# Optimization experiments

Hardware: AMD Instinct MI355X
Metric: run time of the kernel (lower is better)

Reference implementation:

```python
import jax, jax.numpy as jnp
import numpy as np

N, H, D, HDIM, HID = 768, 4, 3, 64, 64


def setup_inputs() -> dict:
    key = jax.random.key(0)
    ks = jax.random.split(key, 12)

    def w(k, shape, scale=None):
        s = (1.0 / np.sqrt(shape[0])) if scale is None else scale
        return (jax.random.normal(k, shape, jnp.float32) * s).astype(jnp.float32)

    d_in_e = H + 2 * (HDIM + H * H)  # 4 + 2*(64+16) = 164
    return {
        "x": jax.random.normal(ks[0], (N, H, D), jnp.float32),
        "h": jax.random.normal(ks[1], (N, HDIM), jnp.float32),
        "phi_e_w0": w(ks[2], (d_in_e, HID)), "phi_e_b0": jnp.zeros((HID,), jnp.float32),
        "phi_e_w1": w(ks[3], (HID, HID)), "phi_e_b1": jnp.zeros((HID,), jnp.float32),
        "phi_inf_w": w(ks[4], (HID, 1)), "phi_inf_b": jnp.zeros((1,), jnp.float32),
        "phi_x_w0": w(ks[5], (HID, HID)), "phi_x_b0": jnp.zeros((HID,), jnp.float32),
        "phi_x_w1": w(ks[6], (HID, HID)), "phi_x_b1": jnp.zeros((HID,), jnp.float32),
        "phi_x_w2": w(ks[7], (HID, H), scale=0.001), "phi_x_b2": jnp.zeros((H,), jnp.float32),
        "phi_h_w0": w(ks[8], (HID + HDIM, HID)), "phi_h_b0": jnp.zeros((HID,), jnp.float32),
        "phi_h_w1": w(ks[9], (HID, HID)), "phi_h_b1": jnp.zeros((HID,), jnp.float32),
        "phi_h_w2": w(ks[10], (HID, HDIM)), "phi_h_b2": jnp.zeros((HDIM,), jnp.float32),
    }


def _mlp2(z, w0, b0, w1, b1):
    # hk.nets.MLP([HID, HID], activation=silu, activate_final=True)
    return jax.nn.silu(jax.nn.silu(z @ w0 + b0) @ w1 + b1)


def reference(x, h,
              phi_e_w0, phi_e_b0, phi_e_w1, phi_e_b1,
              phi_inf_w, phi_inf_b,
              phi_x_w0, phi_x_b0, phi_x_w1, phi_x_b1, phi_x_w2, phi_x_b2,
              phi_h_w0, phi_h_b0, phi_h_w1, phi_h_b1, phi_h_w2, phi_h_b2):
    n, n_heads = x.shape[0], x.shape[1]
    avg_num_neighbours = n - 1
    off_n = 1.0 - jnp.eye(n, dtype=x.dtype)          # zero node-diagonal mask

    # per-node head-pair differences: [n, H, H, 3], entry [m,i,j] = x[m,j]-x[m,i]
    diff_heads = x[:, None, :, :] - x[:, :, None, :]
    sq_norms_heads = jnp.sum(diff_heads ** 2, axis=-1)            # [n, H, H]
    h_concat = jnp.concatenate([h, sq_norms_heads.reshape(n, n_heads * n_heads)], axis=-1)

    # all-pairs node features: [n, n, 2*(HDIM+H^2)], entry [i,j] = [h_concat[j], h_concat[i]]
    hc_dim = h_concat.shape[-1]
    h_combos = jnp.concatenate([
        jnp.broadcast_to(h_concat[None, :, :], (n, n, hc_dim)),
        jnp.broadcast_to(h_concat[:, None, :], (n, n, hc_dim)),
    ], axis=-1)

    # all-pairs node differences per head: [n, n, H, 3], entry [i,j] = x[j]-x[i]
    diff_nodes = x[None, :, :, :] - x[:, None, :, :]
    sq_norms_nodes = jnp.sum(diff_nodes ** 2, axis=-1)            # [n, n, H]

    e_in = jnp.concatenate([sq_norms_nodes, h_combos], axis=-1)   # [n, n, 164]
    m_ij = _mlp2(e_in, phi_e_w0, phi_e_b0, phi_e_w1, phi_e_b1)    # [n, n, HID]
    m_ij = m_ij * off_n[:, :, None]

    e = jax.nn.sigmoid(m_ij @ phi_inf_w + phi_inf_b)[..., 0] * off_n  # [n, n]
    m_i = jnp.einsum('ijd,ij->id', m_ij, e) / jnp.sqrt(jnp.asarray(avg_num_neighbours, x.dtype))

    # phi_x: MLP(silu, activate_final) -> Linear(H) (tanh=False)
    phi_x_out = (_mlp2(m_ij, phi_x_w0, phi_x_b0, phi_x_w1, phi_x_b1) @ phi_x_w2 + phi_x_b2)
    phi_x_out = phi_x_out * off_n[:, :, None]                     # [n, n, H]

    # normalize_by_x_norm=True, normalization_constant=1.0
    norm = jnp.sqrt(jnp.where(sq_norms_nodes == 0.0, 1.0, sq_norms_nodes)) + 1.0
    norm_diff = (diff_nodes / norm[..., None]) * off_n[:, :, None, None]
    equivariant_shift = jnp.einsum('ijhd,ijh->ihd', norm_diff, phi_x_out)
    equivariant_shift = equivariant_shift / avg_num_neighbours    # agg='mean'

    x_new = x + equivariant_shift

    phi_h_in = jnp.concatenate([m_i, h], axis=-1)
    h_new = _mlp2(phi_h_in, phi_h_w0, phi_h_b0, phi_h_w1, phi_h_b1) @ phi_h_w2 + phi_h_b2
    h_new = h + h_new                                             # residual_h=True
    return (x_new, h_new)
```

## Files before the change

### kernel.cpp

```cpp
#include <hip/hip_runtime.h>
#include <hip/hip_bf16.h>
#include <math.h>

#define WS_BJ    0
#define WS_BI    49152
#define WS_W0AT  98304
#define WS_BIAS  98560
#define WS_INFW  98784
#define WS_WG    98848

typedef unsigned short ushort_t;
typedef __attribute__((ext_vector_type(8))) __bf16 bf16x8;
typedef __attribute__((ext_vector_type(4))) float f32x4;

__device__ __forceinline__ float silu_f(float v) {
    return v * __builtin_amdgcn_rcpf(1.0f + __expf(-v));
}
__device__ __forceinline__ float sigm_f(float v) {
    return __builtin_amdgcn_rcpf(1.0f + __expf(-v));
}

__device__ __forceinline__ ushort_t bf16r(float f) {
    unsigned u = __float_as_uint(f);
    u += 0x7FFFu + ((u >> 16) & 1u);
    return (ushort_t)(u >> 16);
}
__device__ __forceinline__ float bf2f(ushort_t s) { return __uint_as_float(((unsigned)s) << 16); }

__device__ __forceinline__ unsigned pk2(float a, float b) {
    __hip_bfloat162 t = __float22bfloat162_rn(make_float2(a, b));
    return *reinterpret_cast<unsigned*>(&t);
}

__global__ __launch_bounds__(64) void prep_kernel(
    const float* __restrict__ x, const float* __restrict__ h,
    const float* __restrict__ ew0, const float* __restrict__ eb0,
    const float* __restrict__ ew1, const float* __restrict__ eb1,
    const float* __restrict__ infw, const float* __restrict__ infb,
    const float* __restrict__ xw0, const float* __restrict__ xb0,
    const float* __restrict__ xw1, const float* __restrict__ xb1,
    const float* __restrict__ xw2, const float* __restrict__ xb2,
    float* __restrict__ ws)
{
    const int blk = blockIdx.x, t = threadIdx.x;
    if (blk < 768) {
        __shared__ float hcs[80];
        const int m = blk;
        hcs[t] = h[m * 64 + t];
        if (t < 16) {
            int i2 = t >> 2, j2 = t & 3;
            float d0 = x[m*12 + j2*3 + 0] - x[m*12 + i2*3 + 0];
            float d1 = x[m*12 + j2*3 + 1] - x[m*12 + i2*3 + 1];
            float d2 = x[m*12 + j2*3 + 2] - x[m*12 + i2*3 + 2];
            hcs[64 + t] = d0*d0 + d1*d1 + d2*d2;
        }
        __syncthreads();
        float bj = 0.0f, bi = eb0[t];
        #pragma unroll 4
        for (int k = 0; k < 80; ++k) {
            float hv = hcs[k];
            bj += hv * ew0[(4 + k) * 64 + t];
            bi += hv * ew0[(84 + k) * 64 + t];
        }
        ws[WS_BJ + m * 64 + t] = bj;
        ws[WS_BI + m * 64 + t] = bi;
    } else if (blk == 768) {
        #pragma unroll
        for (int hh = 0; hh < 4; ++hh) ws[WS_W0AT + t * 4 + hh] = ew0[hh * 64 + t];
        ws[WS_INFW + t] = infw[t];
        #pragma unroll
        for (int u = 0; u < 4; ++u) {
            int idx = u * 64 + t;
            if (idx < 224) {
                float v;
                if (idx < 64)        v = eb1[idx];
                else if (idx < 128)  v = xb0[idx - 64];
                else if (idx == 128) v = infb[0];
                else if (idx < 144)  v = 0.0f;
                else if (idx < 208)  v = xb1[idx - 144];
                else if (idx < 212)  v = xb2[idx - 208];
                else                 v = 0.0f;
                ws[WS_BIAS + idx] = v;
            }
        }
    } else {
        ushort_t* wg = (ushort_t*)(ws + WS_WG);
        #pragma unroll 1
        for (int u = 0; u < 8; ++u) {
            int e = (blk - 769) * 512 + u * 64 + t;
            int r = e >> 6, k = e & 63;
            float v;
            if (r < 64)        v = ew1[k * 64 + r];
            else if (r < 128)  v = xw0[k * 64 + (r - 64)];
            else if (r == 128) v = infw[k];
            else if (r < 144)  v = 0.0f;
            else if (r < 208)  v = xw1[k * 64 + (r - 144)];
            else if (r < 212)  v = xw2[k * 4 + (r - 208)];
            else               v = 0.0f;
            wg[e] = bf16r(v);
        }
    }
}

__device__ __forceinline__ void load_bfrags(const ushort_t* yb, int ml, int q, bf16x8 B[4][2]) {
    #pragma unroll
    for (int pt = 0; pt < 4; ++pt)
        #pragma unroll
        for (int kt = 0; kt < 2; ++kt)
            B[pt][kt] = *(const bf16x8*)(yb + (pt*16 + ml) * 72 + kt*32 + q*8);
}

template<int NMT>
__device__ __forceinline__ void gemmG(const ushort_t* __restrict__ wg, int ml, int q,
                                      const bf16x8 B[4][2], f32x4* acc) {
    #pragma unroll
    for (int mt = 0; mt < NMT; ++mt) {
        #pragma unroll
        for (int kt = 0; kt < 2; ++kt) {
            bf16x8 af = *(const bf16x8*)(wg + (mt*16 + ml) * 64 + kt*32 + q*8);
            #pragma unroll
            for (int pt = 0; pt < 4; ++pt)
                acc[mt*4 + pt] = __builtin_amdgcn_mfma_f32_16x16x32_bf16(af, B[pt][kt], acc[mt*4 + pt], 0, 0, 0);
        }
    }
}

__device__ __forceinline__ void ep_silu2(ushort_t* yb, int ml, int q,
                                         const f32x4* acc, const float* __restrict__ bias,
                                         int coff) {
    #pragma unroll
    for (int mt = 0; mt < 2; ++mt) {
        float4 bv = *(const float4*)(bias + coff + mt*16 + q*4);
        #pragma unroll
        for (int pt = 0; pt < 4; ++pt) {
            f32x4 a = acc[mt*4 + pt];
            uint2 w = make_uint2(pk2(silu_f(a[0] + bv.x), silu_f(a[1] + bv.y)),
                                 pk2(silu_f(a[2] + bv.z), silu_f(a[3] + bv.w)));
            *(uint2*)(yb + (pt*16 + ml) * 72 + coff + mt*16 + q*4) = w;
        }
    }
}

__device__ __forceinline__ void layer64(ushort_t* yb, const ushort_t* __restrict__ wg,
                                        const float* __restrict__ bias, int ml, int q) {
    bf16x8 B[4][2];
    load_bfrags(yb, ml, q, B);
    f32x4 acc[8];
    #pragma unroll
    for (int t = 0; t < 8; ++t) acc[t] = f32x4{0.f, 0.f, 0.f, 0.f};
    gemmG<2>(wg, ml, q, B, acc);
    ep_silu2(yb, ml, q, acc, bias, 0);
    #pragma unroll
    for (int t = 0; t < 8; ++t) acc[t] = f32x4{0.f, 0.f, 0.f, 0.f};
    gemmG<2>(wg + 32*64, ml, q, B, acc);
    ep_silu2(yb, ml, q, acc, bias, 32);
}

__global__ __launch_bounds__(256, 2) void egcl_kernel(
    const float* __restrict__ x, const float* __restrict__ h,
    const float* __restrict__ hw0, const float* __restrict__ hb0,
    const float* __restrict__ hw1, const float* __restrict__ hb1,
    const float* __restrict__ hw2, const float* __restrict__ hb2,
    const float* __restrict__ ws, float* __restrict__ out)
{
    __shared__ ushort_t ybuf[4][4608];
    __shared__ float sbuf[4][64];
    __shared__ float pbuf[4][256];
    __shared__ float redm[4][64];
    __shared__ float reds[4][12];
    __shared__ float inbuf[128];
    __shared__ float zbuf[64];

    const int i = blockIdx.x, tid = threadIdx.x;
    const int wv = tid >> 6, lane = tid & 63;
    const int ml = lane & 15, q = lane >> 4;

    const ushort_t* wg = (const ushort_t*)(ws + WS_WG);
    const float* bias  = ws + WS_BIAS;
    const float* infwf = ws + WS_INFW;

    if (wv == 1) inbuf[64 + lane] = h[i * 64 + lane];
    if (lane < 12) reds[wv][lane] = 0.0f;

    float xi[12];
    #pragma unroll
    for (int t = 0; t < 12; ++t) xi[t] = x[i * 12 + t];

    const float* Bi   = ws + WS_BI + i * 64;
    const float* w0at = ws + WS_W0AT;
    ushort_t* yb = ybuf[wv];

    float macc = 0.0f;

    #pragma unroll 1
    for (int it = 0; it < 3; ++it) {
        const int jg = it * 256 + wv * 64 + lane;

        float sqn[4];
        {
            const float4* xp = (const float4*)(x + jg * 12);
            float4 a = xp[0], b = xp[1], c = xp[2];
            float d0, d1, d2;
            d0=a.x-xi[0]; d1=a.y-xi[1]; d2=a.z-xi[2];   sqn[0]=d0*d0+d1*d1+d2*d2;
            d0=a.w-xi[3]; d1=b.x-xi[4]; d2=b.y-xi[5];   sqn[1]=d0*d0+d1*d1+d2*d2;
            d0=b.z-xi[6]; d1=b.w-xi[7]; d2=c.x-xi[8];   sqn[2]=d0*d0+d1*d1+d2*d2;
            d0=c.y-xi[9]; d1=c.z-xi[10];d2=c.w-xi[11];  sqn[3]=d0*d0+d1*d1+d2*d2;
        }

        {
            const float* Bj = ws + WS_BJ + jg * 64;
            #pragma unroll
            for (int b = 0; b < 8; ++b) {
                float4 A = *(const float4*)(Bj + b*8);
                float4 Bv = *(const float4*)(Bj + b*8 + 4);
                float z[8] = {A.x, A.y, A.z, A.w, Bv.x, Bv.y, Bv.z, Bv.w};
                #pragma unroll
                for (int u = 0; u < 8; ++u) {
                    int l = b*8 + u;
                    float v = Bi[l] + z[u]
                            + sqn[0]*w0at[l*4+0] + sqn[1]*w0at[l*4+1]
                            + sqn[2]*w0at[l*4+2] + sqn[3]*w0at[l*4+3];
                    z[u] = silu_f(v);
                }
                uint4 pkv = make_uint4(pk2(z[0],z[1]), pk2(z[2],z[3]),
                                       pk2(z[4],z[5]), pk2(z[6],z[7]));
                *(uint4*)(yb + lane * 72 + b*8) = pkv;
            }
        }

        layer64(yb, wg + 0, bias + 0, ml, q);

        {
            float sv = bias[128];
            #pragma unroll
            for (int c = 0; c < 8; ++c) {
                uint2 w0 = *(const uint2*)(yb + lane * 72 + c*8);
                uint2 w1 = *(const uint2*)(yb + lane * 72 + c*8 + 4);
                sv += __uint_as_float(w0.x << 16)          * infwf[c*8 + 0];
                sv += __uint_as_float(w0.x & 0xFFFF0000u)  * infwf[c*8 + 1];
                sv += __uint_as_float(w0.y << 16)          * infwf[c*8 + 2];
                sv += __uint_as_float(w0.y & 0xFFFF0000u)  * infwf[c*8 + 3];
                sv += __uint_as_float(w1.x << 16)          * infwf[c*8 + 4];
                sv += __uint_as_float(w1.x & 0xFFFF0000u)  * infwf[c*8 + 5];
                sv += __uint_as_float(w1.y << 16)          * infwf[c*8 + 6];
                sv += __uint_as_float(w1.y & 0xFFFF0000u)  * infwf[c*8 + 7];
            }
            sbuf[wv][lane] = (jg == i) ? 0.0f : sigm_f(sv);
        }

        #pragma unroll 8
        for (int j2 = 0; j2 < 64; ++j2) {
            float ev = sbuf[wv][j2];
            macc += ev * bf2f(yb[j2 * 72 + lane]);
        }

        layer64(yb, wg + 64*64, bias + 64, ml, q);
        layer64(yb, wg + 144*64, bias + 144, ml, q);

        {
            bf16x8 B[4][2];
            load_bfrags(yb, ml, q, B);
            f32x4 acc2[4];
            #pragma unroll
            for (int t = 0; t < 4; ++t) acc2[t] = f32x4{0.f, 0.f, 0.f, 0.f};
            gemmG<1>(wg + 208*64, ml, q, B, acc2);
            if (q == 0) {
                float4 bx2 = *(const float4*)(bias + 208);
                #pragma unroll
                for (int pt = 0; pt < 4; ++pt) {
                    float4 pv = make_float4(acc2[pt][0] + bx2.x, acc2[pt][1] + bx2.y,
                                            acc2[pt][2] + bx2.z, acc2[pt][3] + bx2.w);
                    *(float4*)(pbuf[wv] + (pt*16 + ml) * 4) = pv;
                }
            }
        }

        {
            float4 pv = *(const float4*)(pbuf[wv] + lane * 4);
            float pvh[4] = {pv.x, pv.y, pv.z, pv.w};
            float mask = (jg == i) ? 0.0f : 1.0f;
            const float4* xp = (const float4*)(x + jg * 12);
            float4 a = xp[0], b = xp[1], c = xp[2];
            float dxs[12];
            dxs[0]=a.x-xi[0]; dxs[1]=a.y-xi[1]; dxs[2]=a.z-xi[2];  dxs[3]=a.w-xi[3];
            dxs[4]=b.x-xi[4]; dxs[5]=b.y-xi[5]; dxs[6]=b.z-xi[6];  dxs[7]=b.w-xi[7];
            dxs[8]=c.x-xi[8]; dxs[9]=c.y-xi[9]; dxs[10]=c.z-xi[10];dxs[11]=c.w-xi[11];
            float s12[12];
            #pragma unroll
            for (int hh = 0; hh < 4; ++hh) {
                float nsq = (sqn[hh] == 0.0f) ? 1.0f : sqn[hh];
                float inv = mask * pvh[hh] * __builtin_amdgcn_rcpf(sqrtf(nsq) + 1.0f);
                #pragma unroll
                for (int d = 0; d < 3; ++d)
                    s12[hh*3 + d] = dxs[hh*3 + d] * inv;
            }
            #pragma unroll
            for (int t = 0; t < 12; ++t) {
                float v = s12[t];
                v += __shfl_xor(v, 1, 64);
                v += __shfl_xor(v, 2, 64);
                v += __shfl_xor(v, 4, 64);
                v += __shfl_xor(v, 8, 64);
                v += __shfl_xor(v, 16, 64);
                v += __shfl_xor(v, 32, 64);
                if (lane == 0) reds[wv][t] += v;
            }
        }
    }

    redm[wv][lane] = macc;
    __syncthreads();

    if (wv == 0) {
        float mi = (redm[0][lane] + redm[1][lane] + redm[2][lane] + redm[3][lane])
                   * (1.0f / sqrtf(767.0f));
        inbuf[lane] = mi;

        if (lane < 12) {
            float sh = reds[0][lane] + reds[1][lane] + reds[2][lane] + reds[3][lane];
            out[i*12 + lane] = x[i*12 + lane] + sh * (1.0f / 767.0f);
        }

        float a = hb0[lane];
        #pragma unroll 8
        for (int k = 0; k < 128; ++k) a += inbuf[k] * hw0[k*64 + lane];
        zbuf[lane] = silu_f(a);

        a = hb1[lane];
        #pragma unroll 8
        for (int k = 0; k < 64; ++k) a += zbuf[k] * hw1[k*64 + lane];
        zbuf[lane] = silu_f(a);

        a = hb2[lane];
        #pragma unroll 8
        for (int k = 0; k < 64; ++k) a += zbuf[k] * hw2[k*64 + lane];
        out[9216 + i*64 + lane] = h[i*64 + lane] + a;
    }
}

extern "C" void kernel_launch(void* const* d_in, const int* in_sizes, int n_in,
                              void* d_out, int out_size, void* d_ws, size_t ws_size,
                              hipStream_t stream) {
    const float* x    = (const float*)d_in[0];
    const float* h    = (const float*)d_in[1];
    const float* ew0  = (const float*)d_in[2];
    const float* eb0  = (const float*)d_in[3];
    const float* ew1  = (const float*)d_in[4];
    const float* eb1  = (const float*)d_in[5];
    const float* infw = (const float*)d_in[6];
    const float* infb = (const float*)d_in[7];
    const float* xw0  = (const float*)d_in[8];
    const float* xb0  = (const float*)d_in[9];
    const float* xw1  = (const float*)d_in[10];
    const float* xb1  = (const float*)d_in[11];
    const float* xw2  = (const float*)d_in[12];
    const float* xb2  = (const float*)d_in[13];
    const float* hw0  = (const float*)d_in[14];
    const float* hb0  = (const float*)d_in[15];
    const float* hw1  = (const float*)d_in[16];
    const float* hb1  = (const float*)d_in[17];
    const float* hw2  = (const float*)d_in[18];
    const float* hb2  = (const float*)d_in[19];

    float* ws  = (float*)d_ws;
    float* out = (float*)d_out;

    prep_kernel<<<797, 64, 0, stream>>>(x, h, ew0, eb0, ew1, eb1, infw, infb,
                                        xw0, xb0, xw1, xb1, xw2, xb2, ws);
    egcl_kernel<<<768, 256, 0, stream>>>(x, h, hw0, hb0, hw1, hb1, hw2, hb2, ws, out);
}
```

Before: 203.8 us.

## Split per-node j-loop across blocks and move phi_h MLP to a finish kernel

The main kernel no longer loops three times over 256-neighbour chunks within one block. It launches a 3x768 grid where each block handles one chunk and writes partial m_i and shift sums to workspace. A separate finish kernel reduces the partials and runs the phi_h MLP. The prep kernel is repacked into 256-thread blocks with four nodes each, and the weight-packing store pattern changes. This triples the block count for better CU occupancy and load balance, and takes the serial single-wave tail out of the heavy kernel, at the cost of an extra launch and a workspace round-trip.

```diff
diff --git a/kernel.cpp b/kernel.cpp
--- a/kernel.cpp
+++ b/kernel.cpp
@@ -8,6 +8,8 @@
 #define WS_BIAS  98560
 #define WS_INFW  98784
 #define WS_WG    98848
+#define WS_PM    106016
+#define WS_PS    253472
 
 typedef unsigned short ushort_t;
 typedef __attribute__((ext_vector_type(8))) __bf16 bf16x8;
@@ -32,7 +34,7 @@
     return *reinterpret_cast<unsigned*>(&t);
 }
 
-__global__ __launch_bounds__(64) void prep_kernel(
+__global__ __launch_bounds__(256) void prep_kernel(
     const float* __restrict__ x, const float* __restrict__ h,
     const float* __restrict__ ew0, const float* __restrict__ eb0,
     const float* __restrict__ ew1, const float* __restrict__ eb1,
@@ -42,52 +44,54 @@
     const float* __restrict__ xw2, const float* __restrict__ xb2,
     float* __restrict__ ws)
 {
-    const int blk = blockIdx.x, t = threadIdx.x;
-    if (blk < 768) {
-        __shared__ float hcs[80];
-        const int m = blk;
-        hcs[t] = h[m * 64 + t];
+    const int blk = blockIdx.x, tid = threadIdx.x;
+    const int wv = tid >> 6, t = tid & 63;
+    if (blk < 192) {
+        __shared__ float hcs[4][80];
+        const int m = blk * 4 + wv;
+        hcs[wv][t] = h[m * 64 + t];
         if (t < 16) {
             int i2 = t >> 2, j2 = t & 3;
             float d0 = x[m*12 + j2*3 + 0] - x[m*12 + i2*3 + 0];
             float d1 = x[m*12 + j2*3 + 1] - x[m*12 + i2*3 + 1];
             float d2 = x[m*12 + j2*3 + 2] - x[m*12 + i2*3 + 2];
-            hcs[64 + t] = d0*d0 + d1*d1 + d2*d2;
-        }
-        __syncthreads();
+            hcs[wv][64 + t] = d0*d0 + d1*d1 + d2*d2;
+        }
         float bj = 0.0f, bi = eb0[t];
         #pragma unroll 4
         for (int k = 0; k < 80; ++k) {
-            float hv = hcs[k];
+            float hv = hcs[wv][k];
             bj += hv * ew0[(4 + k) * 64 + t];
             bi += hv * ew0[(84 + k) * 64 + t];
         }
         ws[WS_BJ + m * 64 + t] = bj;
         ws[WS_BI + m * 64 + t] = bi;
-    } else if (blk == 768) {
-        #pragma unroll
-        for (int hh = 0; hh < 4; ++hh) ws[WS_W0AT + t * 4 + hh] = ew0[hh * 64 + t];
-        ws[WS_INFW + t] = infw[t];
-        #pragma unroll
-        for (int u = 0; u < 4; ++u) {
-            int idx = u * 64 + t;
-            if (idx < 224) {
-                float v;
-                if (idx < 64)        v = eb1[idx];
-                else if (idx < 128)  v = xb0[idx - 64];
-                else if (idx == 128) v = infb[0];
-                else if (idx < 144)  v = 0.0f;
-                else if (idx < 208)  v = xb1[idx - 144];
-                else if (idx < 212)  v = xb2[idx - 208];
-                else                 v = 0.0f;
-                ws[WS_BIAS + idx] = v;
+    } else if (blk == 192) {
+        if (wv == 0) {
+            #pragma unroll
+            for (int hh = 0; hh < 4; ++hh) ws[WS_W0AT + t * 4 + hh] = ew0[hh * 64 + t];
+            ws[WS_INFW + t] = infw[t];
+            #pragma unroll
+            for (int u = 0; u < 4; ++u) {
+                int idx = u * 64 + t;
+                if (idx < 224) {
+                    float v;
+                    if (idx < 64)        v = eb1[idx];
+                    else if (idx < 128)  v = xb0[idx - 64];
+                    else if (idx == 128) v = infb[0];
+                    else if (idx < 144)  v = 0.0f;
+                    else if (idx < 208)  v = xb1[idx - 144];
+                    else if (idx < 212)  v = xb2[idx - 208];
+                    else                 v = 0.0f;
+                    ws[WS_BIAS + idx] = v;
+                }
             }
         }
     } else {
         ushort_t* wg = (ushort_t*)(ws + WS_WG);
         #pragma unroll 1
         for (int u = 0; u < 8; ++u) {
-            int e = (blk - 769) * 512 + u * 64 + t;
+            int e = (blk - 193) * 2048 + tid * 8 + u;
             int r = e >> 6, k = e & 63;
             float v;
             if (r < 64)        v = ew1[k * 64 + r];
@@ -156,186 +160,191 @@
     ep_silu2(yb, ml, q, acc, bias, 32);
 }
 
-__global__ __launch_bounds__(256, 2) void egcl_kernel(
+__global__ __launch_bounds__(256, 2) void egcl_chunk(
+    const float* __restrict__ x, float* __restrict__ ws)
+{
+    __shared__ ushort_t ybuf[4][4608];
+    __shared__ float sbuf[4][64];
+    __shared__ float redm[4][64];
+    __shared__ float reds[4][12];
+
+    const int it = blockIdx.x, i = blockIdx.y, tid = threadIdx.x;
+    const int wv = tid >> 6, lane = tid & 63;
+    const int ml = lane & 15, q = lane >> 4;
+    const int jg = it * 256 + wv * 64 + lane;
+
+    const ushort_t* wg = (const ushort_t*)(ws + WS_WG);
+    const float* bias  = ws + WS_BIAS;
+    const float* infwf = ws + WS_INFW;
+    const float* Bi    = ws + WS_BI + i * 64;
+    const float* w0at  = ws + WS_W0AT;
+    ushort_t* yb = ybuf[wv];
+
+    float xi[12];
+    #pragma unroll
+    for (int t = 0; t < 12; ++t) xi[t] = x[i * 12 + t];
+
+    float sqn[4];
+    {
+        const float4* xp = (const float4*)(x + jg * 12);
+        float4 a = xp[0], b = xp[1], c = xp[2];
+        float d0, d1, d2;
+        d0=a.x-xi[0]; d1=a.y-xi[1]; d2=a.z-xi[2];   sqn[0]=d0*d0+d1*d1+d2*d2;
+        d0=a.w-xi[3]; d1=b.x-xi[4]; d2=b.y-xi[5];   sqn[1]=d0*d0+d1*d1+d2*d2;
+        d0=b.z-xi[6]; d1=b.w-xi[7]; d2=c.x-xi[8];   sqn[2]=d0*d0+d1*d1+d2*d2;
+        d0=c.y-xi[9]; d1=c.z-xi[10];d2=c.w-xi[11];  sqn[3]=d0*d0+d1*d1+d2*d2;
+    }
+
+    {
+        const float* Bj = ws + WS_BJ + jg * 64;
+        #pragma unroll
+        for (int b = 0; b < 8; ++b) {
+            float4 A = *(const float4*)(Bj + b*8);
+            float4 Bv = *(const float4*)(Bj + b*8 + 4);
+            float z[8] = {A.x, A.y, A.z, A.w, Bv.x, Bv.y, Bv.z, Bv.w};
+            #pragma unroll
+            for (int u = 0; u < 8; ++u) {
+                int l = b*8 + u;
+                float v = Bi[l] + z[u]
+                        + sqn[0]*w0at[l*4+0] + sqn[1]*w0at[l*4+1]
+                        + sqn[2]*w0at[l*4+2] + sqn[3]*w0at[l*4+3];
+                z[u] = silu_f(v);
+            }
+            uint4 pkv = make_uint4(pk2(z[0],z[1]), pk2(z[2],z[3]),
+                                   pk2(z[4],z[5]), pk2(z[6],z[7]));
+            *(uint4*)(yb + lane * 72 + b*8) = pkv;
+        }
+    }
+
+    layer64(yb, wg + 0, bias + 0, ml, q);
+
+    {
+        float sv = bias[128];
+        #pragma unroll
+        for (int c = 0; c < 8; ++c) {
+            uint2 w0 = *(const uint2*)(yb + lane * 72 + c*8);
+            uint2 w1 = *(const uint2*)(yb + lane * 72 + c*8 + 4);
+            sv += __uint_as_float(w0.x << 16)          * infwf[c*8 + 0];
+            sv += __uint_as_float(w0.x & 0xFFFF0000u)  * infwf[c*8 + 1];
+            sv += __uint_as_float(w0.y << 16)          * infwf[c*8 + 2];
+            sv += __uint_as_float(w0.y & 0xFFFF0000u)  * infwf[c*8 + 3];
+            sv += __uint_as_float(w1.x << 16)          * infwf[c*8 + 4];
+            sv += __uint_as_float(w1.x & 0xFFFF0000u)  * infwf[c*8 + 5];
+            sv += __uint_as_float(w1.y << 16)          * infwf[c*8 + 6];
+            sv += __uint_as_float(w1.y & 0xFFFF0000u)  * infwf[c*8 + 7];
+        }
+        sbuf[wv][lane] = (jg == i) ? 0.0f : sigm_f(sv);
+    }
+
+    float macc = 0.0f;
+    #pragma unroll 8
+    for (int j2 = 0; j2 < 64; ++j2) {
+        float ev = sbuf[wv][j2];
+        macc += ev * bf2f(yb[j2 * 72 + lane]);
+    }
+
+    layer64(yb, wg + 64*64, bias + 64, ml, q);
+    layer64(yb, wg + 144*64, bias + 144, ml, q);
+
+    float* yf = (float*)yb;
+    {
+        bf16x8 B[4][2];
+        load_bfrags(yb, ml, q, B);
+        f32x4 acc2[4];
+        #pragma unroll
+        for (int t = 0; t < 4; ++t) acc2[t] = f32x4{0.f, 0.f, 0.f, 0.f};
+        gemmG<1>(wg + 208*64, ml, q, B, acc2);
+        if (q == 0) {
+            float4 bx2 = *(const float4*)(bias + 208);
+            #pragma unroll
+            for (int pt = 0; pt < 4; ++pt) {
+                float4 pv = make_float4(acc2[pt][0] + bx2.x, acc2[pt][1] + bx2.y,
+                                        acc2[pt][2] + bx2.z, acc2[pt][3] + bx2.w);
+                *(float4*)(yf + (pt*16 + ml) * 4) = pv;
+            }
+        }
+    }
+
+    {
+        float4 pv = *(const float4*)(yf + lane * 4);
+        float pvh[4] = {pv.x, pv.y, pv.z, pv.w};
+        float mask = (jg == i) ? 0.0f : 1.0f;
+        const float4* xp = (const float4*)(x + jg * 12);
+        float4 a = xp[0], b = xp[1], c = xp[2];
+        float dxs[12];
+        dxs[0]=a.x-xi[0]; dxs[1]=a.y-xi[1]; dxs[2]=a.z-xi[2];  dxs[3]=a.w-xi[3];
+        dxs[4]=b.x-xi[4]; dxs[5]=b.y-xi[5]; dxs[6]=b.z-xi[6];  dxs[7]=b.w-xi[7];
+        dxs[8]=c.x-xi[8]; dxs[9]=c.y-xi[9]; dxs[10]=c.z-xi[10];dxs[11]=c.w-xi[11];
+        float s12[12];
+        #pragma unroll
+        for (int hh = 0; hh < 4; ++hh) {
+            float nsq = (sqn[hh] == 0.0f) ? 1.0f : sqn[hh];
+            float inv = mask * pvh[hh] * __builtin_amdgcn_rcpf(sqrtf(nsq) + 1.0f);
+            #pragma unroll
+            for (int d = 0; d < 3; ++d)
+                s12[hh*3 + d] = dxs[hh*3 + d] * inv;
+        }
+        #pragma unroll
+        for (int t = 0; t < 12; ++t) {
+            float v = s12[t];
+            v += __shfl_xor(v, 1, 64);
+            v += __shfl_xor(v, 2, 64);
+            v += __shfl_xor(v, 4, 64);
+            v += __shfl_xor(v, 8, 64);
+            v += __shfl_xor(v, 16, 64);
+            v += __shfl_xor(v, 32, 64);
+            if (lane == 0) reds[wv][t] = v;
+        }
+    }
+
+    redm[wv][lane] = macc;
+    __syncthreads();
+
+    if (wv == 0) {
+        ws[WS_PM + (i*3 + it)*64 + lane] =
+            redm[0][lane] + redm[1][lane] + redm[2][lane] + redm[3][lane];
+        if (lane < 12)
+            ws[WS_PS + (i*3 + it)*12 + lane] =
+                reds[0][lane] + reds[1][lane] + reds[2][lane] + reds[3][lane];
+    }
+}
+
+__global__ __launch_bounds__(64) void finish_kernel(
     const float* __restrict__ x, const float* __restrict__ h,
     const float* __restrict__ hw0, const float* __restrict__ hb0,
     const float* __restrict__ hw1, const float* __restrict__ hb1,
     const float* __restrict__ hw2, const float* __restrict__ hb2,
     const float* __restrict__ ws, float* __restrict__ out)
 {
-    __shared__ ushort_t ybuf[4][4608];
-    __shared__ float sbuf[4][64];
-    __shared__ float pbuf[4][256];
-    __shared__ float redm[4][64];
-    __shared__ float reds[4][12];
     __shared__ float inbuf[128];
     __shared__ float zbuf[64];
-
-    const int i = blockIdx.x, tid = threadIdx.x;
-    const int wv = tid >> 6, lane = tid & 63;
-    const int ml = lane & 15, q = lane >> 4;
-
-    const ushort_t* wg = (const ushort_t*)(ws + WS_WG);
-    const float* bias  = ws + WS_BIAS;
-    const float* infwf = ws + WS_INFW;
-
-    if (wv == 1) inbuf[64 + lane] = h[i * 64 + lane];
-    if (lane < 12) reds[wv][lane] = 0.0f;
-
-    float xi[12];
-    #pragma unroll
-    for (int t = 0; t < 12; ++t) xi[t] = x[i * 12 + t];
-
-    const float* Bi   = ws + WS_BI + i * 64;
-    const float* w0at = ws + WS_W0AT;
-    ushort_t* yb = ybuf[wv];
-
-    float macc = 0.0f;
-
-    #pragma unroll 1
-    for (int it = 0; it < 3; ++it) {
-        const int jg = it * 256 + wv * 64 + lane;
-
-        float sqn[4];
-        {
-            const float4* xp = (const float4*)(x + jg * 12);
-            float4 a = xp[0], b = xp[1], c = xp[2];
-            float d0, d1, d2;
-            d0=a.x-xi[0]; d1=a.y-xi[1]; d2=a.z-xi[2];   sqn[0]=d0*d0+d1*d1+d2*d2;
-            d0=a.w-xi[3]; d1=b.x-xi[4]; d2=b.y-xi[5];   sqn[1]=d0*d0+d1*d1+d2*d2;
-            d0=b.z-xi[6]; d1=b.w-xi[7]; d2=c.x-xi[8];   sqn[2]=d0*d0+d1*d1+d2*d2;
-            d0=c.y-xi[9]; d1=c.z-xi[10];d2=c.w-xi[11];  sqn[3]=d0*d0+d1*d1+d2*d2;
-        }
-
-        {
-            const float* Bj = ws + WS_BJ + jg * 64;
-            #pragma unroll
-            for (int b = 0; b < 8; ++b) {
-                float4 A = *(const float4*)(Bj + b*8);
-                float4 Bv = *(const float4*)(Bj + b*8 + 4);
-                float z[8] = {A.x, A.y, A.z, A.w, Bv.x, Bv.y, Bv.z, Bv.w};
-                #pragma unroll
-                for (int u = 0; u < 8; ++u) {
-                    int l = b*8 + u;
-                    float v = Bi[l] + z[u]
-                            + sqn[0]*w0at[l*4+0] + sqn[1]*w0at[l*4+1]
-                            + sqn[2]*w0at[l*4+2] + sqn[3]*w0at[l*4+3];
-                    z[u] = silu_f(v);
-                }
-                uint4 pkv = make_uint4(pk2(z[0],z[1]), pk2(z[2],z[3]),
-                                       pk2(z[4],z[5]), pk2(z[6],z[7]));
-                *(uint4*)(yb + lane * 72 + b*8) = pkv;
-            }
-        }
-
-        layer64(yb, wg + 0, bias + 0, ml, q);
-
-        {
-            float sv = bias[128];
-            #pragma unroll
-            for (int c = 0; c < 8; ++c) {
-                uint2 w0 = *(const uint2*)(yb + lane * 72 + c*8);
-                uint2 w1 = *(const uint2*)(yb + lane * 72 + c*8 + 4);
-                sv += __uint_as_float(w0.x << 16)          * infwf[c*8 + 0];
-                sv += __uint_as_float(w0.x & 0xFFFF0000u)  * infwf[c*8 + 1];
-                sv += __uint_as_float(w0.y << 16)          * infwf[c*8 + 2];
-                sv += __uint_as_float(w0.y & 0xFFFF0000u)  * infwf[c*8 + 3];
-                sv += __uint_as_float(w1.x << 16)          * infwf[c*8 + 4];
-                sv += __uint_as_float(w1.x & 0xFFFF0000u)  * infwf[c*8 + 5];
-                sv += __uint_as_float(w1.y << 16)          * infwf[c*8 + 6];
-                sv += __uint_as_float(w1.y & 0xFFFF0000u)  * infwf[c*8 + 7];
-            }
-            sbuf[wv][lane] = (jg == i) ? 0.0f : sigm_f(sv);
-        }
-
-        #pragma unroll 8
-        for (int j2 = 0; j2 < 64; ++j2) {
-            float ev = sbuf[wv][j2];
-            macc += ev * bf2f(yb[j2 * 72 + lane]);
-        }
-
-        layer64(yb, wg + 64*64, bias + 64, ml, q);
-        layer64(yb, wg + 144*64, bias + 144, ml, q);
-
-        {
-            bf16x8 B[4][2];
-            load_bfrags(yb, ml, q, B);
-            f32x4 acc2[4];
-            #pragma unroll
-            for (int t = 0; t < 4; ++t) acc2[t] = f32x4{0.f, 0.f, 0.f, 0.f};
-            gemmG<1>(wg + 208*64, ml, q, B, acc2);
-            if (q == 0) {
-                float4 bx2 = *(const float4*)(bias + 208);
-                #pragma unroll
-                for (int pt = 0; pt < 4; ++pt) {
-                    float4 pv = make_float4(acc2[pt][0] + bx2.x, acc2[pt][1] + bx2.y,
-                                            acc2[pt][2] + bx2.z, acc2[pt][3] + bx2.w);
-                    *(float4*)(pbuf[wv] + (pt*16 + ml) * 4) = pv;
-                }
-            }
-        }
-
-        {
-            float4 pv = *(const float4*)(pbuf[wv] + lane * 4);
-            float pvh[4] = {pv.x, pv.y, pv.z, pv.w};
-            float mask = (jg == i) ? 0.0f : 1.0f;
-            const float4* xp = (const float4*)(x + jg * 12);
-            float4 a = xp[0], b = xp[1], c = xp[2];
-            float dxs[12];
-            dxs[0]=a.x-xi[0]; dxs[1]=a.y-xi[1]; dxs[2]=a.z-xi[2];  dxs[3]=a.w-xi[3];
-            dxs[4]=b.x-xi[4]; dxs[5]=b.y-xi[5]; dxs[6]=b.z-xi[6];  dxs[7]=b.w-xi[7];
-            dxs[8]=c.x-xi[8]; dxs[9]=c.y-xi[9]; dxs[10]=c.z-xi[10];dxs[11]=c.w-xi[11];
-            float s12[12];
-            #pragma unroll
-            for (int hh = 0; hh < 4; ++hh) {
-                float nsq = (sqn[hh] == 0.0f) ? 1.0f : sqn[hh];
-                float inv = mask * pvh[hh] * __builtin_amdgcn_rcpf(sqrtf(nsq) + 1.0f);
-                #pragma unroll
-                for (int d = 0; d < 3; ++d)
-                    s12[hh*3 + d] = dxs[hh*3 + d] * inv;
-            }
-            #pragma unroll
-            for (int t = 0; t < 12; ++t) {
-                float v = s12[t];
-                v += __shfl_xor(v, 1, 64);
-                v += __shfl_xor(v, 2, 64);
-                v += __shfl_xor(v, 4, 64);
-                v += __shfl_xor(v, 8, 64);
-                v += __shfl_xor(v, 16, 64);
-                v += __shfl_xor(v, 32, 64);
-                if (lane == 0) reds[wv][t] += v;
-            }
-        }
-    }
-
-    redm[wv][lane] = macc;
-    __syncthreads();
-
-    if (wv == 0) {
-        float mi = (redm[0][lane] + redm[1][lane] + redm[2][lane] + redm[3][lane])
-                   * (1.0f / sqrtf(767.0f));
-        inbuf[lane] = mi;
-
-        if (lane < 12) {
-            float sh = reds[0][lane] + reds[1][lane] + reds[2][lane] + reds[3][lane];
-            out[i*12 + lane] = x[i*12 + lane] + sh * (1.0f / 767.0f);
-        }
-
-        float a = hb0[lane];
-        #pragma unroll 8
-        for (int k = 0; k < 128; ++k) a += inbuf[k] * hw0[k*64 + lane];
-        zbuf[lane] = silu_f(a);
-
-        a = hb1[lane];
-        #pragma unroll 8
-        for (int k = 0; k < 64; ++k) a += zbuf[k] * hw1[k*64 + lane];
-        zbuf[lane] = silu_f(a);
-
-        a = hb2[lane];
-        #pragma unroll 8
-        for (int k = 0; k < 64; ++k) a += zbuf[k] * hw2[k*64 + lane];
-        out[9216 + i*64 + lane] = h[i*64 + lane] + a;
-    }
+    const int i = blockIdx.x, lane = threadIdx.x;
+
+    const float* pm = ws + WS_PM + i*3*64;
+    float mi = (pm[lane] + pm[64 + lane] + pm[128 + lane]) * (1.0f / sqrtf(767.0f));
+    inbuf[lane] = mi;
+    inbuf[64 + lane] = h[i*64 + lane];
+
+    if (lane < 12) {
+        const float* ps = ws + WS_PS + i*3*12;
+        float sh = ps[lane] + ps[12 + lane] + ps[24 + lane];
+        out[i*12 + lane] = x[i*12 + lane] + sh * (1.0f / 767.0f);
+    }
+
+    float a = hb0[lane];
+    #pragma unroll 8
+    for (int k = 0; k < 128; ++k) a += inbuf[k] * hw0[k*64 + lane];
+    zbuf[lane] = silu_f(a);
+
+    a = hb1[lane];
+    #pragma unroll 8
+    for (int k = 0; k < 64; ++k) a += zbuf[k] * hw1[k*64 + lane];
+    zbuf[lane] = silu_f(a);
+
+    a = hb2[lane];
+    #pragma unroll 8
+    for (int k = 0; k < 64; ++k) a += zbuf[k] * hw2[k*64 + lane];
+    out[9216 + i*64 + lane] = h[i*64 + lane] + a;
 }
 
 extern "C" void kernel_launch(void* const* d_in, const int* in_sizes, int n_in,
@@ -365,7 +374,8 @@
     float* ws  = (float*)d_ws;
     float* out = (float*)d_out;
 
-    prep_kernel<<<797, 64, 0, stream>>>(x, h, ew0, eb0, ew1, eb1, infw, infb,
-                                        xw0, xb0, xw1, xb1, xw2, xb2, ws);
-    egcl_kernel<<<768, 256, 0, stream>>>(x, h, hw0, hb0, hw1, hb1, hw2, hb2, ws, out);
-}
+    prep_kernel<<<200, 256, 0, stream>>>(x, h, ew0, eb0, ew1, eb1, infw, infb,
+                                         xw0, xb0, xw1, xb1, xw2, xb2, ws);
+    egcl_chunk<<<dim3(3, 768), 256, 0, stream>>>(x, ws);
+    finish_kernel<<<768, 64, 0, stream>>>(x, h, hw0, hb0, hw1, hb1, hw2, hb2, ws, out);
+}
```

New measurement: 171.0 us. 1.19x faster.
